# Optimization experiments

Hardware: AMD Instinct MI355X
Metric: run time of the kernel (lower is better)

Reference implementation:

```python
import jax, jax.numpy as jnp
import numpy as np

B, L, C, H = 4, 1024, 768, 12
D = C // H  # head_ch = 64


def setup_inputs() -> dict:
    key = jax.random.key(0)
    ks = jax.random.split(key, 8)
    s = 1.0 / np.sqrt(C)
    return {
        "inputs_q": jax.random.normal(ks[0], (B, L, C), jnp.float32),
        "inputs_kv": jax.random.normal(ks[1], (B, L, C), jnp.float32),
        "Wq": jax.random.normal(ks[2], (C, H * D), jnp.float32) * s,
        "Wk": jax.random.normal(ks[3], (C, H * D), jnp.float32) * s,
        "Wv": jax.random.normal(ks[4], (C, H * D), jnp.float32) * s,
        "Wout": jax.random.normal(ks[5], (H * D, C), jnp.float32) * s,
        "W_pre": jax.random.normal(ks[6], (H, H), jnp.float32) * (1.0 / np.sqrt(H)),
        "W_post": jax.random.normal(ks[7], (H, H), jnp.float32) * (1.0 / np.sqrt(H)),
    }


def reference(inputs_q, inputs_kv, Wq, Wk, Wv, Wout, W_pre, W_post):
    # Linear projections (no bias), split into heads: b l (h d) -> b h l d
    def split_heads(x):
        b, l, _ = x.shape
        return x.reshape(b, l, H, D).transpose(0, 2, 1, 3)

    q = split_heads(inputs_q @ Wq) / jnp.sqrt(jnp.asarray(D, inputs_q.dtype))
    k = split_heads(inputs_kv @ Wk)
    v = split_heads(inputs_kv @ Wv)

    # Attention logits [b, h, l, k]
    weights = jnp.einsum('bhld,bhkd->bhlk', q, k)
    # Talking-heads: learned cross-head mixing pre-softmax
    weights = jnp.einsum('bhlk,hi->bilk', weights, W_pre)
    weights = jax.nn.softmax(weights, axis=-1)
    # Talking-heads post-softmax mixing
    weights = jnp.einsum('bhlk,hi->bilk', weights, W_post)

    scores = jnp.einsum('bhlk,bhkd->bhld', weights, v)
    scores = scores.transpose(0, 2, 1, 3).reshape(B, L, H * D)  # b l (h d)
    return scores @ Wout
```

## Files before the change

kernel.cpp:

```cpp
#include <hip/hip_runtime.h>
#include <hip/hip_bf16.h>

#define BB 4
#define LL 1024
#define CC 768
#define HH 12
#define DD 64

typedef unsigned short ushort_t;
typedef __attribute__((ext_vector_type(8))) short bf16x8;
typedef __attribute__((ext_vector_type(4))) float f32x4;
typedef __attribute__((ext_vector_type(2))) float f32x2;

__device__ inline ushort_t f2bf(float x) {
    union { float f; unsigned u; } v; v.f = x;
    unsigned r = (v.u + 0x7FFFu + ((v.u >> 16) & 1u)) >> 16;
    return (ushort_t)r;
}
__device__ inline float u2f(unsigned u) {
    union { unsigned u; float f; } v; v.u = u;
    return v.f;
}
__device__ inline unsigned pack2bf(float lo, float hi) {
    union { __hip_bfloat162 v; unsigned u; } r;
    r.v = __float22bfloat162_rn(make_float2(lo, hi));
    return r.u;
}

__device__ inline void stage_rows(const ushort_t* __restrict__ g, int stride,
                                  ushort_t* lds, int nbytes, int wave, int lane) {
    const int ko = (lane & 3) << 3;
    const int rsub = lane >> 2;
    for (int off = wave * 1024; off < nbytes; off += 4096) {
        int row = (off >> 6) + rsub;
        __builtin_amdgcn_global_load_lds(
            (const __attribute__((address_space(1))) void*)(g + (size_t)row * stride + ko),
            (__attribute__((address_space(3))) void*)(lds + (off >> 1)),
            16, 0, 0);
    }
}

__global__ __launch_bounds__(256) void prep(const float* __restrict__ q, const float* __restrict__ kv,
                                            const float* __restrict__ w0, const float* __restrict__ w1,
                                            const float* __restrict__ w2, const float* __restrict__ w3,
                                            ushort_t* __restrict__ qo, ushort_t* __restrict__ kvo,
                                            ushort_t* __restrict__ o0, ushort_t* __restrict__ o1,
                                            ushort_t* __restrict__ o2, ushort_t* __restrict__ o3,
                                            float* __restrict__ Zp) {
    __shared__ float t[32][33];
    const int bx = blockIdx.x;
    if (bx < 3072) {
        const float* src = bx < 1536 ? q : kv;
        ushort_t* dst = bx < 1536 ? qo : kvo;
        int bb = bx < 1536 ? bx : bx - 1536;
        size_t i = ((size_t)bb * 256 + threadIdx.x) * 8;
        float4 a = *(const float4*)(src + i);
        float4 b = *(const float4*)(src + i + 4);
        ushort_t u[8] = {f2bf(a.x), f2bf(a.y), f2bf(a.z), f2bf(a.w),
                         f2bf(b.x), f2bf(b.y), f2bf(b.z), f2bf(b.w)};
        *(uint4*)(dst + i) = *(uint4*)u;
    } else if (bx < 5376) {
        int w = bx - 3072;
        int z = w / 576, rem = w % 576;
        const float* W = z == 0 ? w0 : z == 1 ? w1 : z == 2 ? w2 : w3;
        ushort_t* Wt   = z == 0 ? o0 : z == 1 ? o1 : z == 2 ? o2 : o3;
        const int c = threadIdx.x & 31, r0 = threadIdx.x >> 5;
        const int kb = (rem / 24) * 32, nb = (rem % 24) * 32;
#pragma unroll
        for (int i = 0; i < 4; ++i)
            t[r0 + 8 * i][c] = W[(size_t)(kb + r0 + 8 * i) * CC + nb + c];
        __syncthreads();
#pragma unroll
        for (int i = 0; i < 4; ++i)
            Wt[(size_t)(nb + r0 + 8 * i) * CC + kb + c] = f2bf(t[c][r0 + 8 * i]);
    } else {
        Zp[(bx - 5376) * 256 + threadIdx.x] = 0.f;
    }
}

__global__ __launch_bounds__(256) void proj_gemm(const ushort_t* __restrict__ Aq,
                                                 const ushort_t* __restrict__ Akv,
                                                 const ushort_t* __restrict__ Wqt,
                                                 const ushort_t* __restrict__ Wkt,
                                                 const ushort_t* __restrict__ Wvt,
                                                 ushort_t* __restrict__ Qo,
                                                 ushort_t* __restrict__ Ko,
                                                 ushort_t* __restrict__ Vto) {
    const int z = blockIdx.z;
    const ushort_t* A  = (z == 0) ? Aq : Akv;
    const ushort_t* Wt = (z == 0) ? Wqt : (z == 1 ? Wkt : Wvt);

    __shared__ __align__(16) ushort_t a_lds[128 * 32];
    __shared__ __align__(16) ushort_t b_lds[128 * 32];

    const int tid = threadIdx.x;
    const int bm = blockIdx.x * 128, bn = blockIdx.y * 128;
    const int wave = tid >> 6, lane = tid & 63;
    const int quad = lane >> 4, lq = lane & 15;
    const int wr = wave >> 1, wc = wave & 1;

    f32x4 acc[4][4] = {};

    for (int k0 = 0; k0 < CC; k0 += 32) {
        stage_rows(A + (size_t)bm * CC + k0, CC, a_lds, 8192, wave, lane);
        stage_rows(Wt + (size_t)bn * CC + k0, CC, b_lds, 8192, wave, lane);
        __syncthreads();
        bf16x8 af[4], bfr[4];
#pragma unroll
        for (int mi = 0; mi < 4; ++mi)
            af[mi] = *(bf16x8*)&a_lds[(wr * 64 + mi * 16 + lq) * 32 + quad * 8];
#pragma unroll
        for (int ni = 0; ni < 4; ++ni)
            bfr[ni] = *(bf16x8*)&b_lds[(wc * 64 + ni * 16 + lq) * 32 + quad * 8];
#pragma unroll
        for (int mi = 0; mi < 4; ++mi)
#pragma unroll
            for (int ni = 0; ni < 4; ++ni)
                acc[mi][ni] = __builtin_amdgcn_mfma_f32_16x16x32_bf16(af[mi], bfr[ni], acc[mi][ni], 0, 0, 0);
        __syncthreads();
    }

    const float scale = (z == 0) ? 0.125f : 1.0f;
#pragma unroll
    for (int mi = 0; mi < 4; ++mi)
#pragma unroll
        for (int ni = 0; ni < 4; ++ni)
#pragma unroll
            for (int r = 0; r < 4; ++r) {
                int row = bm + wr * 64 + mi * 16 + quad * 4 + r;
                int col = bn + wc * 64 + ni * 16 + lq;
                int b = row >> 10, l = row & 1023, h = col >> 6, d = col & 63;
                ushort_t v = f2bf(acc[mi][ni][r] * scale);
                if (z == 0)      Qo[((size_t)(b * HH + h) * LL + l) * DD + d] = v;
                else if (z == 1) Ko[((size_t)(b * HH + h) * LL + l) * DD + d] = v;
                else             Vto[((size_t)(b * HH + h) * DD + d) * LL + l] = v;
            }
}

__global__ __launch_bounds__(256) void qk_premix(const ushort_t* __restrict__ Q,
                                                 const ushort_t* __restrict__ K,
                                                 const float* __restrict__ Wpre,
                                                 ushort_t* __restrict__ E,
                                                 float* __restrict__ Z) {
    __shared__ __align__(16) ushort_t k_lds[2][2048];
    __shared__ __align__(16) ushort_t q_lds[2][2048];

    const int tid = threadIdx.x;
    const int bk = blockIdx.x * 32;
    const int bl = blockIdx.y * 32;
    const int b  = blockIdx.z;
    const int lane = tid & 63, wave = tid >> 6;
    const int quad = lane >> 4, lq = lane & 15;
    const int wr = wave >> 1, wc = wave & 1;

    const int o = tid << 4;
    const int goff = ((o >> 6) & 31) * DD + (o >> 11) * 32 + ((o >> 4) & 3) * 8;
    const ushort_t* Kbase = K + ((size_t)b * HH * LL + bk) * DD;
    const ushort_t* Qbase = Q + ((size_t)b * HH * LL + bl) * DD;

    f32x4 acc[HH] = {};

#define STAGE_QK(h, bf)                                                                             \
    do {                                                                                            \
        __builtin_amdgcn_global_load_lds(                                                           \
            (const __attribute__((address_space(1))) void*)(Kbase + (size_t)(h) * LL * DD + goff),  \
            (__attribute__((address_space(3))) void*)(&k_lds[bf][0] + (o >> 1)), 16, 0, 0);         \
        __builtin_amdgcn_global_load_lds(                                                           \
            (const __attribute__((address_space(1))) void*)(Qbase + (size_t)(h) * LL * DD + goff),  \
            (__attribute__((address_space(3))) void*)(&q_lds[bf][0] + (o >> 1)), 16, 0, 0);         \
    } while (0)

    STAGE_QK(0, 0);
    __syncthreads();
#pragma unroll
    for (int h = 0; h < HH; ++h) {
        const int buf = h & 1;
        if (h < HH - 1) STAGE_QK(h + 1, buf ^ 1);
        bf16x8 a0 = *(bf16x8*)&k_lds[buf][(wr * 16 + lq) * 32 + quad * 8];
        bf16x8 a1 = *(bf16x8*)&k_lds[buf][1024 + (wr * 16 + lq) * 32 + quad * 8];
        bf16x8 b0 = *(bf16x8*)&q_lds[buf][(wc * 16 + lq) * 32 + quad * 8];
        bf16x8 b1 = *(bf16x8*)&q_lds[buf][1024 + (wc * 16 + lq) * 32 + quad * 8];
        acc[h] = __builtin_amdgcn_mfma_f32_16x16x32_bf16(a0, b0, acc[h], 0, 0, 0);
        acc[h] = __builtin_amdgcn_mfma_f32_16x16x32_bf16(a1, b1, acc[h], 0, 0, 0);
        __syncthreads();
    }
#undef STAGE_QK

    unsigned pk[6][4];
#pragma unroll
    for (int i2 = 0; i2 < 6; ++i2) {
        f32x4 m0 = {}, m1 = {};
#pragma unroll
        for (int h = 0; h < HH; ++h) {
            m0 += acc[h] * Wpre[h * HH + 2 * i2];
            m1 += acc[h] * Wpre[h * HH + 2 * i2 + 1];
        }
#pragma unroll
        for (int r = 0; r < 4; ++r)
            pk[i2][r] = pack2bf(__expf(m0[r]), __expf(m1[r]));
    }

    float zp[HH];
#pragma unroll
    for (int i2 = 0; i2 < 6; ++i2) {
        float s0 = 0.f, s1 = 0.f;
#pragma unroll
        for (int r = 0; r < 4; ++r) {
            s0 += u2f(pk[i2][r] << 16);
            s1 += u2f(pk[i2][r] & 0xFFFF0000u);
        }
        zp[2 * i2] = s0; zp[2 * i2 + 1] = s1;
    }
#pragma unroll
    for (int i = 0; i < HH; ++i) {
        zp[i] += __shfl_xor(zp[i], 16);
        zp[i] += __shfl_xor(zp[i], 32);
    }
    if (quad == 0) {
#pragma unroll
        for (int i = 0; i < HH; ++i)
            atomicAdd(&Z[((size_t)b * HH + i) * LL + bl + wc * 16 + lq], zp[i]);
    }

#pragma unroll
    for (int r = 0; r < 4; ++r) {
        ushort_t* ep = E + (((size_t)b * LL + bk + wr * 16 + quad * 4 + r) * LL
                            + bl + wc * 16 + lq) * HH;
        *(uint2*)ep       = make_uint2(pk[0][r], pk[1][r]);
        *(uint2*)(ep + 4) = make_uint2(pk[2][r], pk[3][r]);
        *(uint2*)(ep + 8) = make_uint2(pk[4][r], pk[5][r]);
    }
}

__global__ __launch_bounds__(512) void pv_postmix(const ushort_t* __restrict__ E,
                                                  const ushort_t* __restrict__ Vt,
                                                  const float* __restrict__ Wpost,
                                                  const float* __restrict__ Z,
                                                  ushort_t* __restrict__ att) {
    __shared__ __align__(16) ushort_t v_lds[HH * 64 * 64];
    __shared__ __align__(16) ushort_t p_lds[HH * 16 * 64];

    const int tid = threadIdx.x;
    const int bl = blockIdx.x * 16;
    const int b  = blockIdx.y;
    const int lane = tid & 63, wave = tid >> 6;
    const int quad = lane >> 4, lq = lane & 15;
    const int ig = (wave >> 2) * 6;
    const int wd = wave & 3;
    const int lmix = tid & 15, kp = tid >> 4;

    float invZ[HH];
#pragma unroll
    for (int h = 0; h < HH; ++h)
        invZ[h] = 1.0f / Z[((size_t)b * HH + h) * LL + bl + lmix];

    f32x4 acc[6] = {};

#pragma unroll 1
    for (int kt = 0; kt < 16; ++kt) {
#pragma unroll
        for (int j = 0; j < 12; ++j) {
            const int o = (tid << 4) + (j << 13);
            const int row = o >> 7;
            const int cs = ((o >> 4) & 7) ^ (row & 7);
            const ushort_t* src = Vt + ((size_t)b * HH * 64 + row) * LL + kt * 64 + cs * 8;
            __builtin_amdgcn_global_load_lds(
                (const __attribute__((address_space(1))) void*)src,
                (__attribute__((address_space(3))) void*)(v_lds + (o >> 1)), 16, 0, 0);
        }

        const int kg = kt * 64 + kp * 2;
        const ushort_t* ep = E + (((size_t)b * LL + kg) * LL + bl + lmix) * HH;
        uint2 ua = *(const uint2*)ep;
        uint2 ub = *(const uint2*)(ep + 4);
        uint2 uc = *(const uint2*)(ep + 8);
        uint2 va = *(const uint2*)(ep + (size_t)LL * HH);
        uint2 vb = *(const uint2*)(ep + (size_t)LL * HH + 4);
        uint2 vc = *(const uint2*)(ep + (size_t)LL * HH + 8);
        unsigned w0[6] = {ua.x, ua.y, ub.x, ub.y, uc.x, uc.y};
        unsigned w1[6] = {va.x, va.y, vb.x, vb.y, vc.x, vc.y};

        f32x2 m[HH] = {};
#pragma unroll
        for (int h2 = 0; h2 < 6; ++h2) {
            f32x2 pe, po;
            pe.x = u2f(w0[h2] << 16);           pe.y = u2f(w1[h2] << 16);
            po.x = u2f(w0[h2] & 0xFFFF0000u);   po.y = u2f(w1[h2] & 0xFFFF0000u);
            pe *= invZ[2 * h2];
            po *= invZ[2 * h2 + 1];
#pragma unroll
            for (int i = 0; i < HH; ++i) {
                m[i] += pe * Wpost[(2 * h2) * HH + i];
                m[i] += po * Wpost[(2 * h2 + 1) * HH + i];
            }
        }
        {
            const int cs = (kp >> 2) ^ (lmix & 7);
            unsigned* pw = (unsigned*)p_lds;
#pragma unroll
            for (int i = 0; i < HH; ++i)
                pw[(i * 16 + lmix) * 32 + cs * 4 + (kp & 3)] = pack2bf(m[i].x, m[i].y);
        }
        __syncthreads();

#pragma unroll
        for (int k0 = 0; k0 < 2; ++k0)
#pragma unroll
            for (int ii = 0; ii < 6; ++ii) {
                const int hh = ig + ii;
                const int ch = ((k0 << 2) + quad) ^ (lq & 7);
                bf16x8 pa  = *(bf16x8*)&p_lds[(hh * 16 + lq) * 64 + ch * 8];
                bf16x8 vbf = *(bf16x8*)&v_lds[(hh * 64 + wd * 16 + lq) * 64 + ch * 8];
                acc[ii] = __builtin_amdgcn_mfma_f32_16x16x32_bf16(pa, vbf, acc[ii], 0, 0, 0);
            }
        __syncthreads();
    }

#pragma unroll
    for (int ii = 0; ii < 6; ++ii)
#pragma unroll
        for (int r = 0; r < 4; ++r)
            att[((size_t)b * LL + bl + quad * 4 + r) * CC + (ig + ii) * 64 + wd * 16 + lq] =
                f2bf(acc[ii][r]);
}

__global__ __launch_bounds__(256) void out_gemm(const ushort_t* __restrict__ A,
                                                const ushort_t* __restrict__ Wt,
                                                float* __restrict__ out) {
    __shared__ __align__(16) ushort_t a_lds[128 * 32];
    __shared__ __align__(16) ushort_t b_lds[64 * 32];

    const int tid = threadIdx.x;
    const int bm = blockIdx.x * 128, bn = blockIdx.y * 64;
    const int wave = tid >> 6, lane = tid & 63;
    const int quad = lane >> 4, lq = lane & 15;
    const int wr = wave >> 1, wc = wave & 1;

    f32x4 acc[4][2] = {};

    for (int k0 = 0; k0 < CC; k0 += 32) {
        stage_rows(A + (size_t)bm * CC + k0, CC, a_lds, 8192, wave, lane);
        stage_rows(Wt + (size_t)bn * CC + k0, CC, b_lds, 4096, wave, lane);
        __syncthreads();
        bf16x8 af[4], bfr[2];
#pragma unroll
        for (int mi = 0; mi < 4; ++mi)
            af[mi] = *(bf16x8*)&a_lds[(wr * 64 + mi * 16 + lq) * 32 + quad * 8];
#pragma unroll
        for (int ni = 0; ni < 2; ++ni)
            bfr[ni] = *(bf16x8*)&b_lds[(wc * 32 + ni * 16 + lq) * 32 + quad * 8];
#pragma unroll
        for (int mi = 0; mi < 4; ++mi)
#pragma unroll
            for (int ni = 0; ni < 2; ++ni)
                acc[mi][ni] = __builtin_amdgcn_mfma_f32_16x16x32_bf16(af[mi], bfr[ni], acc[mi][ni], 0, 0, 0);
        __syncthreads();
    }

#pragma unroll
    for (int mi = 0; mi < 4; ++mi)
#pragma unroll
        for (int ni = 0; ni < 2; ++ni)
#pragma unroll
            for (int r = 0; r < 4; ++r) {
                int row = bm + wr * 64 + mi * 16 + quad * 4 + r;
                int col = bn + wc * 32 + ni * 16 + lq;
                out[(size_t)row * CC + col] = acc[mi][ni][r];
            }
}

extern "C" void kernel_launch(void* const* d_in, const int* in_sizes, int n_in,
                              void* d_out, int out_size, void* d_ws, size_t ws_size,
                              hipStream_t stream) {
    const float* inputs_q  = (const float*)d_in[0];
    const float* inputs_kv = (const float*)d_in[1];
    const float* Wq   = (const float*)d_in[2];
    const float* Wk   = (const float*)d_in[3];
    const float* Wv   = (const float*)d_in[4];
    const float* Wout = (const float*)d_in[5];
    const float* Wpre  = (const float*)d_in[6];
    const float* Wpost = (const float*)d_in[7];
    float* out = (float*)d_out;

    const size_t nS   = (size_t)BB * HH * LL * LL;
    const size_t nQKV = (size_t)BB * HH * LL * DD;
    const size_t nW   = (size_t)CC * CC;

    ushort_t* Eb   = (ushort_t*)d_ws;
    ushort_t* Qb   = Eb + nS;
    ushort_t* Kb   = Qb + nQKV;
    ushort_t* Vtb  = Kb + nQKV;
    ushort_t* attb = Vtb + nQKV;
    ushort_t* inq  = attb + nQKV;
    ushort_t* inkv = inq + nQKV;
    ushort_t* Wqt  = inkv + nQKV;
    ushort_t* Wkt  = Wqt + nW;
    ushort_t* Wvt  = Wkt + nW;
    ushort_t* Wot  = Wvt + nW;
    float*    Zb   = (float*)(Wot + nW);

    dim3 blk(256);

    prep<<<dim3(5568), blk, 0, stream>>>(inputs_q, inputs_kv, Wq, Wk, Wv, Wout,
                                         inq, inkv, Wqt, Wkt, Wvt, Wot, Zb);
    proj_gemm<<<dim3(32, 6, 3), blk, 0, stream>>>(inq, inkv, Wqt, Wkt, Wvt, Qb, Kb, Vtb);
    qk_premix<<<dim3(32, 32, BB), blk, 0, stream>>>(Qb, Kb, Wpre, Eb, Zb);
    pv_postmix<<<dim3(LL / 16, BB), dim3(512), 0, stream>>>(Eb, Vtb, Wpost, Zb, attb);
    out_gemm<<<dim3(32, 12), blk, 0, stream>>>(attb, Wot, out);
}
```

Before: 261.5 us.

## Store Q/K in MFMA-fragment layout, load directly, remap grid per XCD, nontemporal E

```diff
diff --git a/kernel.cpp b/kernel.cpp
--- a/kernel.cpp
+++ b/kernel.cpp
@@ -11,6 +11,7 @@
 typedef __attribute__((ext_vector_type(8))) short bf16x8;
 typedef __attribute__((ext_vector_type(4))) float f32x4;
 typedef __attribute__((ext_vector_type(2))) float f32x2;
+typedef __attribute__((ext_vector_type(2))) unsigned u32x2;
 
 __device__ inline ushort_t f2bf(float x) {
     union { float f; unsigned u; } v; v.f = x;
@@ -131,60 +132,50 @@
                 int col = bn + wc * 64 + ni * 16 + lq;
                 int b = row >> 10, l = row & 1023, h = col >> 6, d = col & 63;
                 ushort_t v = f2bf(acc[mi][ni][r] * scale);
-                if (z == 0)      Qo[((size_t)(b * HH + h) * LL + l) * DD + d] = v;
-                else if (z == 1) Ko[((size_t)(b * HH + h) * LL + l) * DD + d] = v;
-                else             Vto[((size_t)(b * HH + h) * DD + d) * LL + l] = v;
+                if (z == 2) {
+                    Vto[((size_t)(b * HH + h) * DD + d) * LL + l] = v;
+                } else {
+                    size_t off = (size_t)(b * HH + h) * (LL * DD)
+                               + (size_t)(((l >> 4) * 8 + (d >> 3)) * 128 + (l & 15) * 8 + (d & 7));
+                    if (z == 0) Qo[off] = v;
+                    else        Ko[off] = v;
+                }
             }
 }
 
-__global__ __launch_bounds__(256) void qk_premix(const ushort_t* __restrict__ Q,
-                                                 const ushort_t* __restrict__ K,
+__global__ __launch_bounds__(256) void qk_premix(const ushort_t* __restrict__ Qf,
+                                                 const ushort_t* __restrict__ Kf,
                                                  const float* __restrict__ Wpre,
                                                  ushort_t* __restrict__ E,
                                                  float* __restrict__ Z) {
-    __shared__ __align__(16) ushort_t k_lds[2][2048];
-    __shared__ __align__(16) ushort_t q_lds[2][2048];
-
     const int tid = threadIdx.x;
-    const int bk = blockIdx.x * 32;
-    const int bl = blockIdx.y * 32;
-    const int b  = blockIdx.z;
     const int lane = tid & 63, wave = tid >> 6;
     const int quad = lane >> 4, lq = lane & 15;
     const int wr = wave >> 1, wc = wave & 1;
 
-    const int o = tid << 4;
-    const int goff = ((o >> 6) & 31) * DD + (o >> 11) * 32 + ((o >> 4) & 3) * 8;
-    const ushort_t* Kbase = K + ((size_t)b * HH * LL + bk) * DD;
-    const ushort_t* Qbase = Q + ((size_t)b * HH * LL + bl) * DD;
+    const int x = blockIdx.x;
+    const int xcd = x & 7;
+    const int b = xcd >> 1;
+    const int s = x >> 3;
+    const int bk = (s & 31) << 5;
+    const int bl = ((((s >> 5) << 1) | (xcd & 1))) << 5;
+
+    const ushort_t* Kp = Kf + (size_t)b * HH * LL * DD
+                       + (size_t)(((bk >> 4) + wr) * 1024 + quad * 128 + lq * 8);
+    const ushort_t* Qp = Qf + (size_t)b * HH * LL * DD
+                       + (size_t)(((bl >> 4) + wc) * 1024 + quad * 128 + lq * 8);
 
     f32x4 acc[HH] = {};
-
-#define STAGE_QK(h, bf)                                                                             \
-    do {                                                                                            \
-        __builtin_amdgcn_global_load_lds(                                                           \
-            (const __attribute__((address_space(1))) void*)(Kbase + (size_t)(h) * LL * DD + goff),  \
-            (__attribute__((address_space(3))) void*)(&k_lds[bf][0] + (o >> 1)), 16, 0, 0);         \
-        __builtin_amdgcn_global_load_lds(                                                           \
-            (const __attribute__((address_space(1))) void*)(Qbase + (size_t)(h) * LL * DD + goff),  \
-            (__attribute__((address_space(3))) void*)(&q_lds[bf][0] + (o >> 1)), 16, 0, 0);         \
-    } while (0)
-
-    STAGE_QK(0, 0);
-    __syncthreads();
 #pragma unroll
     for (int h = 0; h < HH; ++h) {
-        const int buf = h & 1;
-        if (h < HH - 1) STAGE_QK(h + 1, buf ^ 1);
-        bf16x8 a0 = *(bf16x8*)&k_lds[buf][(wr * 16 + lq) * 32 + quad * 8];
-        bf16x8 a1 = *(bf16x8*)&k_lds[buf][1024 + (wr * 16 + lq) * 32 + quad * 8];
-        bf16x8 b0 = *(bf16x8*)&q_lds[buf][(wc * 16 + lq) * 32 + quad * 8];
-        bf16x8 b1 = *(bf16x8*)&q_lds[buf][1024 + (wc * 16 + lq) * 32 + quad * 8];
-        acc[h] = __builtin_amdgcn_mfma_f32_16x16x32_bf16(a0, b0, acc[h], 0, 0, 0);
-        acc[h] = __builtin_amdgcn_mfma_f32_16x16x32_bf16(a1, b1, acc[h], 0, 0, 0);
-        __syncthreads();
-    }
-#undef STAGE_QK
+        const size_t ho = (size_t)h * (LL * DD);
+        bf16x8 ka0 = *(const bf16x8*)(Kp + ho);
+        bf16x8 ka1 = *(const bf16x8*)(Kp + ho + 512);
+        bf16x8 qb0 = *(const bf16x8*)(Qp + ho);
+        bf16x8 qb1 = *(const bf16x8*)(Qp + ho + 512);
+        acc[h] = __builtin_amdgcn_mfma_f32_16x16x32_bf16(ka0, qb0, acc[h], 0, 0, 0);
+        acc[h] = __builtin_amdgcn_mfma_f32_16x16x32_bf16(ka1, qb1, acc[h], 0, 0, 0);
+    }
 
     unsigned pk[6][4];
 #pragma unroll
@@ -226,9 +217,12 @@
     for (int r = 0; r < 4; ++r) {
         ushort_t* ep = E + (((size_t)b * LL + bk + wr * 16 + quad * 4 + r) * LL
                             + bl + wc * 16 + lq) * HH;
-        *(uint2*)ep       = make_uint2(pk[0][r], pk[1][r]);
-        *(uint2*)(ep + 4) = make_uint2(pk[2][r], pk[3][r]);
-        *(uint2*)(ep + 8) = make_uint2(pk[4][r], pk[5][r]);
+        u32x2 s0; s0.x = pk[0][r]; s0.y = pk[1][r];
+        u32x2 s1; s1.x = pk[2][r]; s1.y = pk[3][r];
+        u32x2 s2; s2.x = pk[4][r]; s2.y = pk[5][r];
+        __builtin_nontemporal_store(s0, (u32x2*)ep);
+        __builtin_nontemporal_store(s1, (u32x2*)(ep + 4));
+        __builtin_nontemporal_store(s2, (u32x2*)(ep + 8));
     }
 }
 
@@ -271,12 +265,12 @@
 
         const int kg = kt * 64 + kp * 2;
         const ushort_t* ep = E + (((size_t)b * LL + kg) * LL + bl + lmix) * HH;
-        uint2 ua = *(const uint2*)ep;
-        uint2 ub = *(const uint2*)(ep + 4);
-        uint2 uc = *(const uint2*)(ep + 8);
-        uint2 va = *(const uint2*)(ep + (size_t)LL * HH);
-        uint2 vb = *(const uint2*)(ep + (size_t)LL * HH + 4);
-        uint2 vc = *(const uint2*)(ep + (size_t)LL * HH + 8);
+        u32x2 ua = __builtin_nontemporal_load((const u32x2*)ep);
+        u32x2 ub = __builtin_nontemporal_load((const u32x2*)(ep + 4));
+        u32x2 uc = __builtin_nontemporal_load((const u32x2*)(ep + 8));
+        u32x2 va = __builtin_nontemporal_load((const u32x2*)(ep + (size_t)LL * HH));
+        u32x2 vb = __builtin_nontemporal_load((const u32x2*)(ep + (size_t)LL * HH + 4));
+        u32x2 vc = __builtin_nontemporal_load((const u32x2*)(ep + (size_t)LL * HH + 8));
         unsigned w0[6] = {ua.x, ua.y, ub.x, ub.y, uc.x, uc.y};
         unsigned w1[6] = {va.x, va.y, vb.x, vb.y, vc.x, vc.y};
 
@@ -404,7 +398,7 @@
     prep<<<dim3(5568), blk, 0, stream>>>(inputs_q, inputs_kv, Wq, Wk, Wv, Wout,
                                          inq, inkv, Wqt, Wkt, Wvt, Wot, Zb);
     proj_gemm<<<dim3(32, 6, 3), blk, 0, stream>>>(inq, inkv, Wqt, Wkt, Wvt, Qb, Kb, Vtb);
-    qk_premix<<<dim3(32, 32, BB), blk, 0, stream>>>(Qb, Kb, Wpre, Eb, Zb);
+    qk_premix<<<dim3(4096), blk, 0, stream>>>(Qb, Kb, Wpre, Eb, Zb);
     pv_postmix<<<dim3(LL / 16, BB), dim3(512), 0, stream>>>(Eb, Vtb, Wpost, Zb, attb);
     out_gemm<<<dim3(32, 12), blk, 0, stream>>>(attb, Wot, out);
 }
```

Measured after the change: 251.8 us. 1.04x faster.
